# Optimization experiments

Measured on AMD Instinct MI355X. Metric: run time of the kernel, lower is better.

## Reference

```python
import jax, jax.numpy as jnp
from jax import lax
import numpy as np


def setup_inputs() -> dict:
    key = jax.random.key(0)
    x = jax.random.normal(key, (16, 1, 1536, 1536), dtype=jnp.float32)
    weight = jnp.ones((1, 1, 3, 3), dtype=jnp.float32) / 9.0
    return {"x": x, "weight": weight}


def _box3x3(z, weight):
    # z: (N, 1, H, W); zero padding=1 (torch conv2d default pad mode)
    return lax.conv_general_dilated(
        z, weight, window_strides=(1, 1), padding=((1, 1), (1, 1)),
        dimension_numbers=("NCHW", "OIHW", "NCHW"))


def _eig2x2(Axx, Axy, Ayy):
    # closed-form eigendecomposition of [[Axx, Axy], [Axy, Ayy]]
    T = Axx + Ayy
    D = Axx * Ayy - Axy * Axy
    s = jnp.sqrt(jnp.abs(T * T * 0.25 - D))
    l1 = T * 0.5 + s
    l2 = T * 0.5 - s
    e11 = l1 - Ayy
    e12 = Axy
    e21 = l2 - Ayy
    e22 = Axy
    small = jnp.abs(Axy) < 1e-9
    e11 = jnp.where(small, 1.0, e11)
    e12 = jnpp_zero = jnp.where(small, 0.0, e12)
    e21 = jnp.where(small, 0.0, e21)
    e22 = jnp.where(small, 1.0, e22)
    # sort so that the eigenvalue with smaller magnitude comes first
    lt = jnp.abs(l1) < jnp.abs(l2)
    lambda1 = jnp.where(lt, l1, l2)
    lambda2 = jnp.where(lt, l2, l1)
    e11_ = jnp.where(lt, e11, e21)
    e12_ = jnp.where(lt, e12, e22)
    e21_ = jnp.where(lt, e21, e11)
    e22_ = jnp.where(lt, e22, e12)
    # NOTE: original torch code has a typo (`labmda2_`), so only lambda1 gets ReLU
    lambda1 = jax.nn.relu(lambda1)
    return lambda1, lambda2, e11_, e12_, e21_, e22_


def reference(x, weight):
    n, c, h, w = x.shape
    # gx[..., 0] = x[..., 1] - x[..., 0]; gx[..., j] = x[..., j-1] - x[..., j]
    gx = jnp.concatenate([x[:, :, :, 1:2], x[:, :, :, :-1]], axis=3) - x
    gy = jnp.concatenate([x[:, :, 1:2, :], x[:, :, :-1, :]], axis=2) - x
    # per-channel box filter then mean over channels (c == 1 here)
    def smooth(z):
        zf = z.reshape(n * c, 1, h, w)
        out = _box3x3(zf, weight).reshape(n, c, h, w)
        return jnp.mean(out, axis=1)  # (N, H, W)
    Axx = smooth(gx * gx)
    Axy = smooth(gx * gy)
    Ayy = smooth(gy * gy)
    return _eig2x2(Axx, Axy, Ayy)
```

## Files before the change

kernel.cpp:

```cpp
#include <hip/hip_runtime.h>


typedef float f32x4 __attribute__((ext_vector_type(4)));
typedef float f32x2 __attribute__((ext_vector_type(2)));

constexpr int N_ = 16, H = 1536, W = 1536;
constexpr int TH = 16, TW = 128;
constexpr int XR = TH + 3;
constexpr int XQ = 34;
constexpr int XC = XQ * 4;

__device__ __forceinline__ void eig_emit(
    const float Sxx[6], const float Sxy[6], const float Syy[6],
    f32x4& o_l1, f32x4& o_l2, f32x4& o_e11, f32x4& o_e12, f32x4& o_e21, f32x4& o_e22) {
    const float inv9 = 1.0f / 9.0f;
#pragma unroll
    for (int k = 0; k < 4; ++k) {
        const float Axx = (Sxx[k] + Sxx[k + 1] + Sxx[k + 2]) * inv9;
        const float Axy = (Sxy[k] + Sxy[k + 1] + Sxy[k + 2]) * inv9;
        const float Ayy = (Syy[k] + Syy[k + 1] + Syy[k + 2]) * inv9;

        const float T  = Axx + Ayy;
        const float Dd = Axx * Ayy - Axy * Axy;
        const float s  = sqrtf(fabsf(T * T * 0.25f - Dd));
        const float l1 = T * 0.5f + s;
        const float l2 = T * 0.5f - s;

        float e11 = l1 - Ayy, e12 = Axy;
        float e21 = l2 - Ayy, e22 = Axy;
        const bool small = fabsf(Axy) < 1e-9f;
        e11 = small ? 1.0f : e11;
        e12 = small ? 0.0f : e12;
        e21 = small ? 0.0f : e21;
        e22 = small ? 1.0f : e22;

        const bool lt = fabsf(l1) < fabsf(l2);
        o_l1[k]  = fmaxf(lt ? l1 : l2, 0.0f);
        o_l2[k]  = lt ? l2 : l1;
        o_e11[k] = lt ? e11 : e21;
        o_e12[k] = lt ? e12 : e22;
        o_e21[k] = lt ? e21 : e11;
        o_e22[k] = lt ? e22 : e12;
    }
}

__global__ __launch_bounds__(256, 5)
void lsa_kernel(const float* __restrict__ x, float* __restrict__ out) {
    __shared__ float Xs[XR][XC];

    const int tj0 = blockIdx.x * TW;
    const int ti0 = blockIdx.y * TH;
    const int n   = blockIdx.z;
    const float* __restrict__ xn = x + (size_t)n * (H * W);
    const int tid  = threadIdx.x;
    const int rsub = tid >> 5;
    const int csub = tid & 31;
    const int cj   = 4 * csub;

    for (int rr = rsub; rr < XR; rr += 8) {
        const int p = ti0 - 2 + rr;
        const float* rowp = xn + (size_t)p * W;
        const bool prow = (p >= 0) & (p < H);
        for (int cq = csub; cq < XQ; cq += 32) {
            const int qb = tj0 - 4 + 4 * cq;
            f32x4 v;
            if (prow && qb >= 0 && qb + 3 < W) {
                v = *reinterpret_cast<const f32x4*>(rowp + qb);
            } else {
                v.x = (prow && qb + 0 >= 0 && qb + 0 < W) ? rowp[qb + 0] : 0.f;
                v.y = (prow && qb + 1 >= 0 && qb + 1 < W) ? rowp[qb + 1] : 0.f;
                v.z = (prow && qb + 2 >= 0 && qb + 2 < W) ? rowp[qb + 2] : 0.f;
                v.w = (prow && qb + 3 >= 0 && qb + 3 < W) ? rowp[qb + 3] : 0.f;
            }
            *reinterpret_cast<f32x4*>(&Xs[rr][4 * cq]) = v;
        }
    }
    __syncthreads();

    const size_t HW = (size_t)H * W;
    const size_t PLANE = (size_t)N_ * HW;
    float* const ob = out + (size_t)n * HW + (size_t)tj0 + cj;

    const bool interior = (ti0 >= 2) & (ti0 <= H - TH - 1) & (tj0 >= 2) & (tj0 <= W - TW - 2);

    if (interior) {
#pragma unroll
        for (int rv = 0; rv < 2; ++rv) {
            const int rr = rsub + 8 * rv;
            float xv[4][7];
#pragma unroll
            for (int dr = 0; dr < 4; ++dr) {
                const f32x2 a = *reinterpret_cast<const f32x2*>(&Xs[rr + dr][cj + 2]);
                const f32x4 b = *reinterpret_cast<const f32x4*>(&Xs[rr + dr][cj + 4]);
                xv[dr][0] = a.x; xv[dr][1] = a.y;
                xv[dr][2] = b.x; xv[dr][3] = b.y; xv[dr][4] = b.z; xv[dr][5] = b.w;
                xv[dr][6] = Xs[rr + dr][cj + 8];
            }
            float Sxx[6], Sxy[6], Syy[6];
#pragma unroll
            for (int m = 0; m < 6; ++m) {
                float sxx = 0.f, sxy = 0.f, syy = 0.f;
#pragma unroll
                for (int d = 0; d < 3; ++d) {
                    const float xc = xv[d + 1][m + 1];
                    const float xl = xv[d + 1][m];
                    const float xu = xv[d][m + 1];
                    const float gx = xl - xc;
                    const float gy = xu - xc;
                    sxx = fmaf(gx, gx, sxx);
                    sxy = fmaf(gx, gy, sxy);
                    syy = fmaf(gy, gy, syy);
                }
                Sxx[m] = sxx; Sxy[m] = sxy; Syy[m] = syy;
            }
            f32x4 o1, o2, o3, o4, o5, o6;
            eig_emit(Sxx, Sxy, Syy, o1, o2, o3, o4, o5, o6);
            float* op = ob + (size_t)(ti0 + rr) * W;
            __builtin_nontemporal_store(o1, reinterpret_cast<f32x4*>(op));
            __builtin_nontemporal_store(o2, reinterpret_cast<f32x4*>(op + PLANE));
            __builtin_nontemporal_store(o3, reinterpret_cast<f32x4*>(op + 2 * PLANE));
            __builtin_nontemporal_store(o4, reinterpret_cast<f32x4*>(op + 3 * PLANE));
            __builtin_nontemporal_store(o5, reinterpret_cast<f32x4*>(op + 4 * PLANE));
            __builtin_nontemporal_store(o6, reinterpret_cast<f32x4*>(op + 5 * PLANE));
        }
    } else {
#pragma unroll
        for (int rv = 0; rv < 2; ++rv) {
            const int rr = rsub + 8 * rv;
            float Sxx[6], Sxy[6], Syy[6];
#pragma unroll
            for (int m = 0; m < 6; ++m) {
                const int q = tj0 + cj - 1 + m;
                float sxx = 0.f, sxy = 0.f, syy = 0.f;
                if (q >= 0 && q < W) {
                    const int cc = cj + m + 3;
#pragma unroll
                    for (int d = 0; d < 3; ++d) {
                        const int p = ti0 + rr - 1 + d;
                        if (p >= 0 && p < H) {
                            const int RR = rr + d + 1;
                            const float xc = Xs[RR][cc];
                            const float xl = (q == 0) ? Xs[RR][cc + 1] : Xs[RR][cc - 1];
                            const float xu = (p == 0) ? Xs[RR + 1][cc] : Xs[RR - 1][cc];
                            const float gx = xl - xc;
                            const float gy = xu - xc;
                            sxx = fmaf(gx, gx, sxx);
                            sxy = fmaf(gx, gy, sxy);
                            syy = fmaf(gy, gy, syy);
                        }
                    }
                }
                Sxx[m] = sxx; Sxy[m] = sxy; Syy[m] = syy;
            }
            f32x4 o1, o2, o3, o4, o5, o6;
            eig_emit(Sxx, Sxy, Syy, o1, o2, o3, o4, o5, o6);
            float* op = ob + (size_t)(ti0 + rr) * W;
            __builtin_nontemporal_store(o1, reinterpret_cast<f32x4*>(op));
            __builtin_nontemporal_store(o2, reinterpret_cast<f32x4*>(op + PLANE));
            __builtin_nontemporal_store(o3, reinterpret_cast<f32x4*>(op + 2 * PLANE));
            __builtin_nontemporal_store(o4, reinterpret_cast<f32x4*>(op + 3 * PLANE));
            __builtin_nontemporal_store(o5, reinterpret_cast<f32x4*>(op + 4 * PLANE));
            __builtin_nontemporal_store(o6, reinterpret_cast<f32x4*>(op + 5 * PLANE));
        }
    }
}

extern "C" void kernel_launch(void* const* d_in, const int* in_sizes, int n_in,
                              void* d_out, int out_size, void* d_ws, size_t ws_size,
                              hipStream_t stream) {
    const float* x = (const float*)d_in[0];
    float* out = (float*)d_out;

    dim3 grid(W / TW, H / TH, N_);
    dim3 block(256);
    lsa_kernel<<<grid, block, 0, stream>>>(x, out);
}
```

Baseline: 181.9 us.

## Replace LDS tile staging with direct per-thread global halo loads

Removes the shared-memory tile and barrier. Each thread now loads its 4x8 input window directly from global memory and relies on L1/L2 to absorb the overlapping halo reads between neighbouring threads. Blocks shrink to 4 rows by 256 columns with one output row per thread. This trades LDS traffic and synchronisation for redundant global and cache loads; the kernel stays dominated by the output write bandwidth.

```diff
diff --git a/kernel.cpp b/kernel.cpp
--- a/kernel.cpp
+++ b/kernel.cpp
@@ -5,14 +5,81 @@
 typedef float f32x2 __attribute__((ext_vector_type(2)));
 
 constexpr int N_ = 16, H = 1536, W = 1536;
-constexpr int TH = 16, TW = 128;
-constexpr int XR = TH + 3;
-constexpr int XQ = 34;
-constexpr int XC = XQ * 4;
 
-__device__ __forceinline__ void eig_emit(
-    const float Sxx[6], const float Sxy[6], const float Syy[6],
-    f32x4& o_l1, f32x4& o_l2, f32x4& o_e11, f32x4& o_e12, f32x4& o_e21, f32x4& o_e22) {
+__global__ __launch_bounds__(256, 4)
+void lsa_kernel(const float* __restrict__ x, float* __restrict__ out) {
+    const int tid  = threadIdx.x;
+    const int rsub = tid >> 6;
+    const int csub = tid & 63;
+    const int ti0  = blockIdx.y * 4;
+    const int tj0  = blockIdx.x * 256;
+    const int n    = blockIdx.z;
+    const int p0   = ti0 + rsub;
+    const int q0   = tj0 + 4 * csub;
+
+    const size_t HW = (size_t)H * W;
+    const size_t PLANE = (size_t)N_ * HW;
+    const float* __restrict__ xn = x + (size_t)n * HW;
+
+    float Sxx[6], Sxy[6], Syy[6];
+    const bool interior = (p0 >= 2) & (p0 <= H - 2) & (q0 >= 2) & (q0 <= W - 6);
+
+    if (interior) {
+        float xv[4][8];
+        const float* rp = xn + (size_t)(p0 - 2) * W + (q0 - 2);
+#pragma unroll
+        for (int d = 0; d < 4; ++d) {
+            const f32x2 a = *reinterpret_cast<const f32x2*>(rp);
+            const f32x4 b = *reinterpret_cast<const f32x4*>(rp + 2);
+            const f32x2 c = *reinterpret_cast<const f32x2*>(rp + 6);
+            xv[d][0] = a.x; xv[d][1] = a.y;
+            xv[d][2] = b.x; xv[d][3] = b.y; xv[d][4] = b.z; xv[d][5] = b.w;
+            xv[d][6] = c.x; xv[d][7] = c.y;
+            rp += W;
+        }
+#pragma unroll
+        for (int m = 0; m < 6; ++m) {
+            float sxx = 0.f, sxy = 0.f, syy = 0.f;
+#pragma unroll
+            for (int d = 0; d < 3; ++d) {
+                const float xc = xv[d + 1][m + 1];
+                const float xl = xv[d + 1][m];
+                const float xu = xv[d][m + 1];
+                const float gx = xl - xc;
+                const float gy = xu - xc;
+                sxx = fmaf(gx, gx, sxx);
+                sxy = fmaf(gx, gy, sxy);
+                syy = fmaf(gy, gy, syy);
+            }
+            Sxx[m] = sxx; Sxy[m] = sxy; Syy[m] = syy;
+        }
+    } else {
+#pragma unroll
+        for (int m = 0; m < 6; ++m) {
+            const int q = q0 - 1 + m;
+            float sxx = 0.f, sxy = 0.f, syy = 0.f;
+            if (q >= 0 && q < W) {
+#pragma unroll
+                for (int d = 0; d < 3; ++d) {
+                    const int p = p0 - 1 + d;
+                    if (p >= 0 && p < H) {
+                        const float* prow = xn + (size_t)p * W;
+                        const float xc = prow[q];
+                        const float xl = (q == 0) ? prow[1] : prow[q - 1];
+                        const float xu = (p == 0) ? xn[(size_t)W + q] : prow[q - W];
+                        const float gx = xl - xc;
+                        const float gy = xu - xc;
+                        sxx = fmaf(gx, gx, sxx);
+                        sxy = fmaf(gx, gy, sxy);
+                        syy = fmaf(gy, gy, syy);
+                    }
+                }
+            }
+            Sxx[m] = sxx; Sxy[m] = sxy; Syy[m] = syy;
+        }
+    }
+
+    f32x4 o_l1, o_l2, o_e11, o_e12, o_e21, o_e22;
     const float inv9 = 1.0f / 9.0f;
 #pragma unroll
     for (int k = 0; k < 4; ++k) {
@@ -42,127 +109,14 @@
         o_e21[k] = lt ? e21 : e11;
         o_e22[k] = lt ? e22 : e12;
     }
-}
 
-__global__ __launch_bounds__(256, 5)
-void lsa_kernel(const float* __restrict__ x, float* __restrict__ out) {
-    __shared__ float Xs[XR][XC];
-
-    const int tj0 = blockIdx.x * TW;
-    const int ti0 = blockIdx.y * TH;
-    const int n   = blockIdx.z;
-    const float* __restrict__ xn = x + (size_t)n * (H * W);
-    const int tid  = threadIdx.x;
-    const int rsub = tid >> 5;
-    const int csub = tid & 31;
-    const int cj   = 4 * csub;
-
-    for (int rr = rsub; rr < XR; rr += 8) {
-        const int p = ti0 - 2 + rr;
-        const float* rowp = xn + (size_t)p * W;
-        const bool prow = (p >= 0) & (p < H);
-        for (int cq = csub; cq < XQ; cq += 32) {
-            const int qb = tj0 - 4 + 4 * cq;
-            f32x4 v;
-            if (prow && qb >= 0 && qb + 3 < W) {
-                v = *reinterpret_cast<const f32x4*>(rowp + qb);
-            } else {
-                v.x = (prow && qb + 0 >= 0 && qb + 0 < W) ? rowp[qb + 0] : 0.f;
-                v.y = (prow && qb + 1 >= 0 && qb + 1 < W) ? rowp[qb + 1] : 0.f;
-                v.z = (prow && qb + 2 >= 0 && qb + 2 < W) ? rowp[qb + 2] : 0.f;
-                v.w = (prow && qb + 3 >= 0 && qb + 3 < W) ? rowp[qb + 3] : 0.f;
-            }
-            *reinterpret_cast<f32x4*>(&Xs[rr][4 * cq]) = v;
-        }
-    }
-    __syncthreads();
-
-    const size_t HW = (size_t)H * W;
-    const size_t PLANE = (size_t)N_ * HW;
-    float* const ob = out + (size_t)n * HW + (size_t)tj0 + cj;
-
-    const bool interior = (ti0 >= 2) & (ti0 <= H - TH - 1) & (tj0 >= 2) & (tj0 <= W - TW - 2);
-
-    if (interior) {
-#pragma unroll
-        for (int rv = 0; rv < 2; ++rv) {
-            const int rr = rsub + 8 * rv;
-            float xv[4][7];
-#pragma unroll
-            for (int dr = 0; dr < 4; ++dr) {
-                const f32x2 a = *reinterpret_cast<const f32x2*>(&Xs[rr + dr][cj + 2]);
-                const f32x4 b = *reinterpret_cast<const f32x4*>(&Xs[rr + dr][cj + 4]);
-                xv[dr][0] = a.x; xv[dr][1] = a.y;
-                xv[dr][2] = b.x; xv[dr][3] = b.y; xv[dr][4] = b.z; xv[dr][5] = b.w;
-                xv[dr][6] = Xs[rr + dr][cj + 8];
-            }
-            float Sxx[6], Sxy[6], Syy[6];
-#pragma unroll
-            for (int m = 0; m < 6; ++m) {
-                float sxx = 0.f, sxy = 0.f, syy = 0.f;
-#pragma unroll
-                for (int d = 0; d < 3; ++d) {
-                    const float xc = xv[d + 1][m + 1];
-                    const float xl = xv[d + 1][m];
-                    const float xu = xv[d][m + 1];
-                    const float gx = xl - xc;
-                    const float gy = xu - xc;
-                    sxx = fmaf(gx, gx, sxx);
-                    sxy = fmaf(gx, gy, sxy);
-                    syy = fmaf(gy, gy, syy);
-                }
-                Sxx[m] = sxx; Sxy[m] = sxy; Syy[m] = syy;
-            }
-            f32x4 o1, o2, o3, o4, o5, o6;
-            eig_emit(Sxx, Sxy, Syy, o1, o2, o3, o4, o5, o6);
-            float* op = ob + (size_t)(ti0 + rr) * W;
-            __builtin_nontemporal_store(o1, reinterpret_cast<f32x4*>(op));
-            __builtin_nontemporal_store(o2, reinterpret_cast<f32x4*>(op + PLANE));
-            __builtin_nontemporal_store(o3, reinterpret_cast<f32x4*>(op + 2 * PLANE));
-            __builtin_nontemporal_store(o4, reinterpret_cast<f32x4*>(op + 3 * PLANE));
-            __builtin_nontemporal_store(o5, reinterpret_cast<f32x4*>(op + 4 * PLANE));
-            __builtin_nontemporal_store(o6, reinterpret_cast<f32x4*>(op + 5 * PLANE));
-        }
-    } else {
-#pragma unroll
-        for (int rv = 0; rv < 2; ++rv) {
-            const int rr = rsub + 8 * rv;
-            float Sxx[6], Sxy[6], Syy[6];
-#pragma unroll
-            for (int m = 0; m < 6; ++m) {
-                const int q = tj0 + cj - 1 + m;
-                float sxx = 0.f, sxy = 0.f, syy = 0.f;
-                if (q >= 0 && q < W) {
-                    const int cc = cj + m + 3;
-#pragma unroll
-                    for (int d = 0; d < 3; ++d) {
-                        const int p = ti0 + rr - 1 + d;
-                        if (p >= 0 && p < H) {
-                            const int RR = rr + d + 1;
-                            const float xc = Xs[RR][cc];
-                            const float xl = (q == 0) ? Xs[RR][cc + 1] : Xs[RR][cc - 1];
-                            const float xu = (p == 0) ? Xs[RR + 1][cc] : Xs[RR - 1][cc];
-                            const float gx = xl - xc;
-                            const float gy = xu - xc;
-                            sxx = fmaf(gx, gx, sxx);
-                            sxy = fmaf(gx, gy, sxy);
-                            syy = fmaf(gy, gy, syy);
-                        }
-                    }
-                }
-                Sxx[m] = sxx; Sxy[m] = sxy; Syy[m] = syy;
-            }
-            f32x4 o1, o2, o3, o4, o5, o6;
-            eig_emit(Sxx, Sxy, Syy, o1, o2, o3, o4, o5, o6);
-            float* op = ob + (size_t)(ti0 + rr) * W;
-            __builtin_nontemporal_store(o1, reinterpret_cast<f32x4*>(op));
-            __builtin_nontemporal_store(o2, reinterpret_cast<f32x4*>(op + PLANE));
-            __builtin_nontemporal_store(o3, reinterpret_cast<f32x4*>(op + 2 * PLANE));
-            __builtin_nontemporal_store(o4, reinterpret_cast<f32x4*>(op + 3 * PLANE));
-            __builtin_nontemporal_store(o5, reinterpret_cast<f32x4*>(op + 4 * PLANE));
-            __builtin_nontemporal_store(o6, reinterpret_cast<f32x4*>(op + 5 * PLANE));
-        }
-    }
+    float* op = out + (size_t)n * HW + (size_t)p0 * W + q0;
+    __builtin_nontemporal_store(o_l1,  reinterpret_cast<f32x4*>(op));
+    __builtin_nontemporal_store(o_l2,  reinterpret_cast<f32x4*>(op + PLANE));
+    __builtin_nontemporal_store(o_e11, reinterpret_cast<f32x4*>(op + 2 * PLANE));
+    __builtin_nontemporal_store(o_e12, reinterpret_cast<f32x4*>(op + 3 * PLANE));
+    __builtin_nontemporal_store(o_e21, reinterpret_cast<f32x4*>(op + 4 * PLANE));
+    __builtin_nontemporal_store(o_e22, reinterpret_cast<f32x4*>(op + 5 * PLANE));
 }
 
 extern "C" void kernel_launch(void* const* d_in, const int* in_sizes, int n_in,
@@ -171,7 +125,7 @@
     const float* x = (const float*)d_in[0];
     float* out = (float*)d_out;
 
-    dim3 grid(W / TW, H / TH, N_);
+    dim3 grid(W / 256, H / 4, N_);
     dim3 block(256);
     lsa_kernel<<<grid, block, 0, stream>>>(x, out);
 }
```

Result: no change. 179.8 us (-1.2%).
